# Kernel tuning notes

Measured on AMD Instinct MI355X. Metric: run time of the kernel, lower is better.

Reference implementation:

```python
import jax, jax.numpy as jnp
import numpy as np

D_MODEL, D_STATE, D_CONV, D_INNER, DT_RANK = 1024, 16, 4, 2048, 64
BATCH, LENGTH = 4, 2048


def setup_inputs() -> dict:
    key = jax.random.key(0)
    ks = jax.random.split(key, 10)
    dt_init_std = DT_RANK ** -0.5
    # dt_proj bias init: inverse-softplus of dt sampled log-uniform in [dt_min, dt_max]
    dt_min, dt_max, dt_floor = 0.001, 0.1, 1e-4
    u = jax.random.uniform(ks[9], (D_INNER,))
    dt = jnp.clip(jnp.exp(u * (np.log(dt_max) - np.log(dt_min)) + np.log(dt_min)), dt_floor, None)
    b_dt = dt + jnp.log(-jnp.expm1(-dt))
    return {
        "x": jax.random.normal(ks[0], (BATCH, LENGTH, D_MODEL), jnp.float32),
        "W_in": jax.random.normal(ks[1], (2 * D_INNER, D_MODEL), jnp.float32) * D_MODEL ** -0.5,
        "conv_w": jax.random.normal(ks[2], (D_INNER, 1, D_CONV), jnp.float32) * D_CONV ** -0.5,
        "conv_b": jax.random.normal(ks[3], (D_INNER,), jnp.float32) * 0.01,
        "W_x": jax.random.normal(ks[4], (DT_RANK + 2 * D_STATE, D_INNER), jnp.float32) * D_INNER ** -0.5,
        "W_dt": jax.random.uniform(ks[5], (D_INNER, DT_RANK), jnp.float32, -dt_init_std, dt_init_std),
        "b_dt": b_dt.astype(jnp.float32),
        "A_raw": jax.random.normal(ks[6], (D_STATE, D_INNER), jnp.float32),
        "D": jax.random.normal(ks[7], (D_INNER,), jnp.float32),
        "W_out": jax.random.normal(ks[8], (D_MODEL, D_INNER), jnp.float32) * D_INNER ** -0.5,
    }


def _mamba_fwd(x, W_in, conv_w, conv_b, W_x, W_dt, b_dt, A_raw, D, W_out):
    b, l, _ = x.shape
    d_inner = W_in.shape[0] // 2
    d_state = A_raw.shape[0]
    dt_rank = W_dt.shape[1]
    xz = jnp.einsum('bld,ed->ble', x, W_in)            # (b, l, 2*d_inner)
    xc, z = jnp.split(xz, 2, axis=-1)
    # causal depthwise conv (torch pads both sides by d_conv-1 then keeps first l == left pad)
    xc = xc.transpose(0, 2, 1)                          # (b, d, l)
    k = conv_w.shape[-1]
    xc = jax.lax.conv_general_dilated(
        xc, conv_w, (1,), [(k - 1, 0)],
        dimension_numbers=('NCH', 'OIH', 'NCH'),
        feature_group_count=d_inner) + conv_b[None, :, None]
    xc = jax.nn.silu(xc).transpose(0, 2, 1)             # (b, l, d)
    dbc = jnp.einsum('bld,ed->ble', xc, W_x)            # (b, l, dt_rank+2*d_state)
    dt, B, C = jnp.split(dbc, [dt_rank, dt_rank + d_state], axis=-1)
    delta = jax.nn.softplus(jnp.einsum('blr,dr->bld', dt, W_dt) + b_dt)  # (b, l, d)
    A = -jnp.exp(A_raw)                                 # (n, d), negative real

    def step(h, inp):
        x_t, dlt, B_t, C_t = inp                        # (b,d),(b,d),(b,n),(b,n)
        dA = jnp.exp(dlt[:, None, :] * A[None])          # (b, n, d)
        h = dA * h + (dlt[:, None, :] * B_t[:, :, None]) * x_t[:, None, :]
        y_t = jnp.einsum('bn,bnd->bd', C_t, h) + D * x_t
        return h, y_t

    h0 = jnp.zeros((b, d_state, d_inner), x.dtype)
    xs = (xc.transpose(1, 0, 2), delta.transpose(1, 0, 2),
          B.transpose(1, 0, 2), C.transpose(1, 0, 2))
    _, ys = jax.lax.scan(step, h0, xs)                  # (l, b, d)
    y = ys.transpose(1, 0, 2) * jax.nn.silu(z)
    return jnp.einsum('bld,md->blm', y, W_out)


def reference(x, W_in, conv_w, conv_b, W_x, W_dt, b_dt, A_raw, D, W_out):
    return _mamba_fwd(x, W_in, conv_w, conv_b, W_x, W_dt, b_dt, A_raw, D, W_out)
```

## Files before the change

### kernel.cpp

```cpp
#include <hip/hip_runtime.h>
#include <hip/hip_bf16.h>

typedef __bf16 bf16;
typedef __bf16 bf16x4 __attribute__((ext_vector_type(4)));
typedef __bf16 bf16x8 __attribute__((ext_vector_type(8)));
typedef float f32x4 __attribute__((ext_vector_type(4)));

__device__ __forceinline__ float fast_exp2(float x) {
#if __has_builtin(__builtin_amdgcn_exp2f)
    return __builtin_amdgcn_exp2f(x);
#else
    return exp2f(x);
#endif
}

__device__ __forceinline__ float fast_log(float x) {
#if __has_builtin(__builtin_amdgcn_logf)
    return __builtin_amdgcn_logf(x) * 0.6931471805599453f;
#else
    return __logf(x);
#endif
}

__device__ __forceinline__ void gload16(bf16* lds, const bf16* g) {
    __builtin_amdgcn_global_load_lds(
        (const __attribute__((address_space(1))) void*)g,
        (__attribute__((address_space(3))) void*)lds,
        16, 0, 0);
}

__device__ __forceinline__ bf16x8 cvt8(const float* p) {
    float4 a = *(const float4*)p;
    float4 b = *(const float4*)(p + 4);
    bf16x8 r;
    r[0] = (bf16)a.x; r[1] = (bf16)a.y; r[2] = (bf16)a.z; r[3] = (bf16)a.w;
    r[4] = (bf16)b.x; r[5] = (bf16)b.y; r[6] = (bf16)b.z; r[7] = (bf16)b.w;
    return r;
}

__global__ __launch_bounds__(256) void cvt_bf16(
    const float* __restrict__ in, bf16* __restrict__ out, int n8)
{
    int i = blockIdx.x * 256 + threadIdx.x;
    if (i < n8)
        *(bf16x8*)(out + (size_t)i * 8) = cvt8(in + (size_t)i * 8);
}

__global__ __launch_bounds__(256) void cvt_all(
    const float* __restrict__ x,  const float* __restrict__ W_in,
    const float* __restrict__ W_x, const float* __restrict__ W_dt,
    bf16* __restrict__ xb, bf16* __restrict__ Wlo, bf16* __restrict__ Whi,
    bf16* __restrict__ Wxb, bf16* __restrict__ Wdtb)
{
    int i = blockIdx.x * 256 + threadIdx.x;
    if (i < 1048576) {
        *(bf16x8*)(xb + (size_t)i * 8) = cvt8(x + (size_t)i * 8);
    } else if (i < 1310720) {
        int j = i - 1048576;
        *(bf16x8*)(Wlo + (size_t)j * 8) = cvt8(W_in + (size_t)j * 8);
    } else if (i < 1572864) {
        int j = i - 1310720;
        *(bf16x8*)(Whi + (size_t)j * 8) = cvt8(W_in + 2097152 + (size_t)j * 8);
    } else if (i < 1597440) {
        int j = i - 1572864;
        *(bf16x8*)(Wxb + (size_t)j * 8) = cvt8(W_x + (size_t)j * 8);
    } else if (i < 1613824) {
        int j = i - 1597440;
        *(bf16x8*)(Wdtb + (size_t)j * 8) = cvt8(W_dt + (size_t)j * 8);
    }
}

template <int EPI, typename TC>
__global__ __launch_bounds__(256, 2) void gemm_bt(
    const bf16* __restrict__ A, int lda,
    const bf16* __restrict__ B, int ldb,
    TC* __restrict__ C, int ldc,
    int K, int Neff, const float* __restrict__ bias,
    const bf16* __restrict__ gmul, size_t zstride)
{
    __shared__ bf16 As0[128 * 32];
    __shared__ bf16 As1[128 * 32];
    __shared__ bf16 Bs0[128 * 32];
    __shared__ bf16 Bs1[128 * 32];

    const int tid  = threadIdx.x;
    const int lane = tid & 63;
    const int wave = tid >> 6;
    const int quad = lane >> 4;
    const int l16  = lane & 15;
    const int wm   = (wave >> 1) << 6;
    const int wn   = (wave & 1) << 6;
    const int bm   = blockIdx.x << 7;
    const int bn   = blockIdx.y << 7;
    const int kb   = blockIdx.z * K;

    const int srow = (wave << 4) + (lane >> 2);
    const int scol = (lane & 3) << 3;

    const bf16* Ag0 = A + (size_t)(bm + srow) * lda + kb + scol;
    const bf16* Ag1 = Ag0 + (size_t)lda * 64;
    int br0 = bn + srow;      br0 = br0 < Neff ? br0 : Neff - 1;
    int br1 = bn + srow + 64; br1 = br1 < Neff ? br1 : Neff - 1;
    const bf16* Bg0 = B + (size_t)br0 * ldb + kb + scol;
    const bf16* Bg1 = B + (size_t)br1 * ldb + kb + scol;

    const int wofs = wave * 512;

    f32x4 acc[4][4] = {};

    for (int k0 = 0; k0 < K; k0 += 64) {
        if (k0) __syncthreads();
        gload16(As0 + wofs,        Ag0 + k0);
        gload16(As0 + 2048 + wofs, Ag1 + k0);
        gload16(Bs0 + wofs,        Bg0 + k0);
        gload16(Bs0 + 2048 + wofs, Bg1 + k0);
        gload16(As1 + wofs,        Ag0 + k0 + 32);
        gload16(As1 + 2048 + wofs, Ag1 + k0 + 32);
        gload16(Bs1 + wofs,        Bg0 + k0 + 32);
        gload16(Bs1 + 2048 + wofs, Bg1 + k0 + 32);
        __syncthreads();

#pragma unroll
        for (int kk = 0; kk < 2; ++kk) {
            const bf16* Ak = kk ? As1 : As0;
            const bf16* Bk = kk ? Bs1 : Bs0;
            bf16x8 af[4], bfr[4];
#pragma unroll
            for (int i = 0; i < 4; ++i) {
                af[i]  = *(const bf16x8*)(Ak + (wm + i * 16 + l16) * 32 + quad * 8);
                bfr[i] = *(const bf16x8*)(Bk + (wn + i * 16 + l16) * 32 + quad * 8);
            }
#pragma unroll
            for (int mi = 0; mi < 4; ++mi)
#pragma unroll
                for (int ni = 0; ni < 4; ++ni)
                    acc[mi][ni] = __builtin_amdgcn_mfma_f32_16x16x32_bf16(
                        af[mi], bfr[ni], acc[mi][ni], 0, 0, 0);
        }
    }

    TC* Cz = C + (size_t)blockIdx.z * zstride;

#pragma unroll
    for (int mi = 0; mi < 4; ++mi) {
        const int row = bm + wm + mi * 16 + quad * 4;
#pragma unroll
        for (int ni = 0; ni < 4; ++ni) {
            const int col = bn + wn + ni * 16 + l16;
            if (col < Neff) {
                float bc = (EPI == 1) ? bias[col] : 0.f;
#pragma unroll
                for (int r = 0; r < 4; ++r) {
                    float v = acc[mi][ni][r];
                    if (EPI == 1) {
                        v += bc;
                        float sp = fast_log(1.f + __expf(v));
                        v = (v > 15.f) ? v : sp;
                    } else if (EPI == 2) {
                        float g = v / (1.f + __expf(-v));
                        v = (float)gmul[(size_t)(row + r) * ldc + col] * g;
                    }
                    Cz[(size_t)(row + r) * ldc + col] = (TC)v;
                }
            }
        }
    }
}

__global__ __launch_bounds__(256) void reduce_split(
    const float* __restrict__ P, bf16* __restrict__ dtb,
    float* __restrict__ BCf)
{
    const size_t base = ((size_t)blockIdx.x * 256 + threadIdx.x) * 4;
    f32x4 s = *(const f32x4*)(P + base);
#pragma unroll
    for (int z = 1; z < 4; ++z) {
        f32x4 p = *(const f32x4*)(P + (size_t)z * 786432 + base);
        s[0] += p[0]; s[1] += p[1]; s[2] += p[2]; s[3] += p[3];
    }
    const int row = (int)(base / 96);
    const int col = (int)(base % 96);
    if (col < 64) {
        bf16x4 o;
        o[0] = (bf16)s[0]; o[1] = (bf16)s[1];
        o[2] = (bf16)s[2]; o[3] = (bf16)s[3];
        *(bf16x4*)(dtb + (size_t)row * 64 + col) = o;
    } else {
        *(f32x4*)(BCf + (size_t)row * 32 + (col - 64)) = s;
    }
}

__global__ __launch_bounds__(256) void conv_kernel(
    const bf16* __restrict__ xh, const float* __restrict__ cw,
    const float* __restrict__ cb, bf16* __restrict__ xc)
{
    const int t0 = blockIdx.x << 3;
    const int b  = blockIdx.y;
    const int d  = threadIdx.x * 8;

    float4 wv[8];
#pragma unroll
    for (int i = 0; i < 8; ++i)
        wv[i] = *(const float4*)(cw + (d + i) * 4);

    float4 cb0 = *(const float4*)(cb + d);
    float4 cb1 = *(const float4*)(cb + d + 4);

    float acc[8][8];
#pragma unroll
    for (int k = 0; k < 8; ++k) {
        acc[k][0] = cb0.x; acc[k][1] = cb0.y; acc[k][2] = cb0.z; acc[k][3] = cb0.w;
        acc[k][4] = cb1.x; acc[k][5] = cb1.y; acc[k][6] = cb1.z; acc[k][7] = cb1.w;
    }

    const bf16* base = xh + ((size_t)b * 2048 + t0) * 2048 + d;

#pragma unroll
    for (int r = 0; r < 11; ++r) {
        const int t_in = t0 - 3 + r;
        if (t_in >= 0) {
            bf16x8 v = *(const bf16x8*)(base + (size_t)(r - 3) * 2048);
            float vf[8];
#pragma unroll
            for (int i = 0; i < 8; ++i) vf[i] = (float)v[i];
#pragma unroll
            for (int j = 0; j < 4; ++j) {
                const int local = r - j;
                if (local >= 0 && local < 8) {
#pragma unroll
                    for (int i = 0; i < 8; ++i) {
                        float w = (j == 0) ? wv[i].x : (j == 1) ? wv[i].y
                                : (j == 2) ? wv[i].z : wv[i].w;
                        acc[local][i] += w * vf[i];
                    }
                }
            }
        }
    }

    bf16* ob = xc + ((size_t)b * 2048 + t0) * 2048 + d;
#pragma unroll
    for (int k = 0; k < 8; ++k) {
        bf16x8 o;
#pragma unroll
        for (int i = 0; i < 8; ++i) {
            float s = acc[k][i];
            o[i] = (bf16)(s / (1.f + __expf(-s)));
        }
        *(bf16x8*)(ob + (size_t)k * 2048) = o;
    }
}

__global__ __launch_bounds__(256, 4) void scan_p1(
    const bf16* __restrict__ delta, const float* __restrict__ BCf,
    const float* __restrict__ A_raw, const bf16* __restrict__ xc,
    bf16* __restrict__ Hb, float* __restrict__ sdtb)
{
    const int d = (blockIdx.x << 8) + threadIdx.x;
    const int b = blockIdx.y;
    const int c = blockIdx.z;

    float A2[16];
#pragma unroll
    for (int n = 0; n < 16; ++n)
        A2[n] = -__expf(A_raw[n * 2048 + d]) * 1.44269504f;

    float h[16];
#pragma unroll
    for (int n = 0; n < 16; ++n) h[n] = 0.f;
    float sdt = 0.f;

    const size_t xbase = ((size_t)(b * 2048 + c * 32)) * 2048 + d;
    const bf16* xp = xc + xbase;
    const bf16* dp = delta + xbase;
    const float* bp = BCf + (size_t)(b * 2048 + c * 32) * 32;

    bf16 xr = xp[0], dr = dp[0];
    f32x4 B0 = *(const f32x4*)(bp);
    f32x4 B1 = *(const f32x4*)(bp + 4);
    f32x4 B2 = *(const f32x4*)(bp + 8);
    f32x4 B3 = *(const f32x4*)(bp + 12);

#pragma unroll 4
    for (int t = 0; t < 32; ++t) {
        const float x  = (float)xr;
        const float dt = (float)dr;
        const f32x4 Ba = B0, Bb = B1, Bc = B2, Bd = B3;
        if (t < 31) {
            xr = xp[(size_t)(t + 1) * 2048];
            dr = dp[(size_t)(t + 1) * 2048];
            const float* nb = bp + (size_t)(t + 1) * 32;
            B0 = *(const f32x4*)nb;
            B1 = *(const f32x4*)(nb + 4);
            B2 = *(const f32x4*)(nb + 8);
            B3 = *(const f32x4*)(nb + 12);
        }
        const float dx = dt * x;
        sdt += dt;
#pragma unroll
        for (int n = 0; n < 4; ++n) {
            float e = fast_exp2(dt * A2[n]);
            h[n] = e * h[n] + Ba[n] * dx;
        }
#pragma unroll
        for (int n = 0; n < 4; ++n) {
            float e = fast_exp2(dt * A2[n + 4]);
            h[n + 4] = e * h[n + 4] + Bb[n] * dx;
        }
#pragma unroll
        for (int n = 0; n < 4; ++n) {
            float e = fast_exp2(dt * A2[n + 8]);
            h[n + 8] = e * h[n + 8] + Bc[n] * dx;
        }
#pragma unroll
        for (int n = 0; n < 4; ++n) {
            float e = fast_exp2(dt * A2[n + 12]);
            h[n + 12] = e * h[n + 12] + Bd[n] * dx;
        }
    }

    const size_t hbase = (((size_t)b * 64 + c) * 2048 + d) * 16;
    bf16x8 h0, h1;
#pragma unroll
    for (int n = 0; n < 8; ++n) {
        h0[n] = (bf16)h[n];
        h1[n] = (bf16)h[n + 8];
    }
    *(bf16x8*)(Hb + hbase) = h0;
    *(bf16x8*)(Hb + hbase + 8) = h1;
    sdtb[((size_t)b * 64 + c) * 2048 + d] = sdt;
}

__global__ __launch_bounds__(256) void scan_p2(
    bf16* __restrict__ Hb, const float* __restrict__ sdtb,
    const float* __restrict__ A_raw)
{
    const int id  = blockIdx.x * 256 + threadIdx.x;
    const int b   = id >> 15;
    const int rem = id & 32767;
    const int d   = rem >> 4;
    const int n   = rem & 15;

    const float A2 = -__expf(A_raw[n * 2048 + d]) * 1.44269504f;
    const size_t hb = (size_t)b * 64 * 32768 + rem;
    const size_t sb = (size_t)b * 64 * 2048 + d;

    float ht = (float)Hb[hb];
#pragma unroll 4
    for (int c = 1; c < 64; ++c) {
        float Hv = (float)Hb[hb + (size_t)c * 32768];
        float a  = fast_exp2(A2 * sdtb[sb + (size_t)c * 2048]);
        ht = Hv + a * ht;
        Hb[hb + (size_t)c * 32768] = (bf16)ht;
    }
}

__global__ __launch_bounds__(256, 4) void scan_p3(
    const bf16* __restrict__ delta, const float* __restrict__ BCf,
    const float* __restrict__ A_raw, const float* __restrict__ Dvec,
    const bf16* __restrict__ Hb, const bf16* xc, bf16* ry)
{
    const int d = (blockIdx.x << 8) + threadIdx.x;
    const int b = blockIdx.y;
    const int c = blockIdx.z;

    float A2[16];
#pragma unroll
    for (int n = 0; n < 16; ++n)
        A2[n] = -__expf(A_raw[n * 2048 + d]) * 1.44269504f;
    const float Dd = Dvec[d];

    float h[16];
    if (c > 0) {
        const bf16* Hp = Hb + (((size_t)b * 64 + (c - 1)) * 2048 + d) * 16;
        bf16x8 v0 = *(const bf16x8*)Hp;
        bf16x8 v1 = *(const bf16x8*)(Hp + 8);
#pragma unroll
        for (int n = 0; n < 8; ++n) {
            h[n]     = (float)v0[n];
            h[n + 8] = (float)v1[n];
        }
    } else {
#pragma unroll
        for (int n = 0; n < 16; ++n) h[n] = 0.f;
    }

    const size_t xbase = ((size_t)(b * 2048 + c * 32)) * 2048 + d;
    const bf16* xp = xc + xbase;
    const bf16* dp = delta + xbase;
    const float* bp = BCf + (size_t)(b * 2048 + c * 32) * 32;
    bf16* yp = ry + xbase;

    bf16 xr = xp[0], dr = dp[0];
    f32x4 B0 = *(const f32x4*)(bp);
    f32x4 B1 = *(const f32x4*)(bp + 4);
    f32x4 B2 = *(const f32x4*)(bp + 8);
    f32x4 B3 = *(const f32x4*)(bp + 12);
    f32x4 C0 = *(const f32x4*)(bp + 16);
    f32x4 C1 = *(const f32x4*)(bp + 20);
    f32x4 C2 = *(const f32x4*)(bp + 24);
    f32x4 C3 = *(const f32x4*)(bp + 28);

#pragma unroll 4
    for (int t = 0; t < 32; ++t) {
        const float x  = (float)xr;
        const float dt = (float)dr;
        const f32x4 Ba = B0, Bb = B1, Bc = B2, Bd = B3;
        const f32x4 Ca = C0, Cb = C1, Cc = C2, Cd = C3;
        if (t < 31) {
            xr = xp[(size_t)(t + 1) * 2048];
            dr = dp[(size_t)(t + 1) * 2048];
            const float* nb = bp + (size_t)(t + 1) * 32;
            B0 = *(const f32x4*)nb;
            B1 = *(const f32x4*)(nb + 4);
            B2 = *(const f32x4*)(nb + 8);
            B3 = *(const f32x4*)(nb + 12);
            C0 = *(const f32x4*)(nb + 16);
            C1 = *(const f32x4*)(nb + 20);
            C2 = *(const f32x4*)(nb + 24);
            C3 = *(const f32x4*)(nb + 28);
        }
        const float dx = dt * x;
        float y = Dd * x;
#pragma unroll
        for (int n = 0; n < 4; ++n) {
            float e = fast_exp2(dt * A2[n]);
            h[n] = e * h[n] + Ba[n] * dx;
            y += Ca[n] * h[n];
        }
#pragma unroll
        for (int n = 0; n < 4; ++n) {
            float e = fast_exp2(dt * A2[n + 4]);
            h[n + 4] = e * h[n + 4] + Bb[n] * dx;
            y += Cb[n] * h[n + 4];
        }
#pragma unroll
        for (int n = 0; n < 4; ++n) {
            float e = fast_exp2(dt * A2[n + 8]);
            h[n + 8] = e * h[n + 8] + Bc[n] * dx;
            y += Cc[n] * h[n + 8];
        }
#pragma unroll
        for (int n = 0; n < 4; ++n) {
            float e = fast_exp2(dt * A2[n + 12]);
            h[n + 12] = e * h[n + 12] + Bd[n] * dx;
            y += Cd[n] * h[n + 12];
        }
        yp[(size_t)t * 2048] = (bf16)y;
    }
}

extern "C" void kernel_launch(void* const* d_in, const int* in_sizes, int n_in,
                              void* d_out, int out_size, void* d_ws, size_t ws_size,
                              hipStream_t stream)
{
    const float* x      = (const float*)d_in[0];
    const float* W_in   = (const float*)d_in[1];
    const float* conv_w = (const float*)d_in[2];
    const float* conv_b = (const float*)d_in[3];
    const float* W_x    = (const float*)d_in[4];
    const float* W_dt   = (const float*)d_in[5];
    const float* b_dt   = (const float*)d_in[6];
    const float* A_raw  = (const float*)d_in[7];
    const float* Dvec   = (const float*)d_in[8];
    const float* W_out  = (const float*)d_in[9];
    float* out = (float*)d_out;

    char* ws = (char*)d_ws;
    bf16*  buf0   = (bf16*)(ws + 0);
    bf16*  buf1   = (bf16*)(ws + 33554432);
    char*  dob    = (char*)d_out;
    bf16*  dtb    = (bf16*)dob;
    float* BCf    = (float*)(dob + 1048576);
    bf16*  xb1    = (bf16*)(dob + 2097152);
    float* Pbuf   = (float*)(dob + 2097152);
    bf16*  Hb     = (bf16*)(dob + 2097152);
    bf16*  xb2    = (bf16*)(dob + 2097152);
    float* sdtb   = (float*)(dob + 18874368);
    bf16*  Whi    = (bf16*)(dob + 20971520);
    bf16*  Wxb    = (bf16*)(dob + 25165824);
    bf16*  Wdtb   = (bf16*)(dob + 25690112);
    bf16*  Wlo    = buf1;
    bf16*  Woutb  = buf1;

    cvt_all<<<dim3(6304), 256, 0, stream>>>(
        x, W_in, W_x, W_dt, xb1, Wlo, Whi, Wxb, Wdtb);

    gemm_bt<0, bf16><<<dim3(64, 16), 256, 0, stream>>>(
        xb1, 1024, Wlo, 1024, buf0, 2048, 1024, 2048, nullptr, nullptr, 0);
    conv_kernel<<<dim3(256, 4), 256, 0, stream>>>(buf0, conv_w, conv_b, buf1);
    gemm_bt<0, float><<<dim3(64, 1, 4), 256, 0, stream>>>(
        buf1, 2048, Wxb, 2048, Pbuf, 96, 512, 96, nullptr, nullptr, 786432);
    reduce_split<<<dim3(768), 256, 0, stream>>>(Pbuf, dtb, BCf);
    gemm_bt<1, bf16><<<dim3(64, 16), 256, 0, stream>>>(
        dtb, 64, Wdtb, 64, buf0, 2048, 64, 2048, b_dt, nullptr, 0);
    scan_p1<<<dim3(8, 4, 64), 256, 0, stream>>>(
        buf0, BCf, A_raw, buf1, Hb, sdtb);
    scan_p2<<<dim3(512), 256, 0, stream>>>(Hb, sdtb, A_raw);
    scan_p3<<<dim3(8, 4, 64), 256, 0, stream>>>(
        buf0, BCf, A_raw, Dvec, Hb, buf1, buf1);
    cvt_bf16<<<dim3(4096), 256, 0, stream>>>(x, xb2, 1048576);
    gemm_bt<2, bf16><<<dim3(64, 16), 256, 0, stream>>>(
        xb2, 1024, Whi, 1024, buf0, 2048, 1024, 2048, nullptr, buf1, 0);
    cvt_bf16<<<dim3(1024), 256, 0, stream>>>(W_out, Woutb, 262144);
    gemm_bt<0, float><<<dim3(64, 8), 256, 0, stream>>>(
        buf0, 2048, Woutb, 2048, out, 1024, 2048, 1024, nullptr, nullptr, 0);
}
```

Before: 417.3 us.

## Add 256x256-tile double-buffered MFMA GEMM for the two input projections

Adds a new 512-thread GEMM kernel using 256x256 output tiles and a 64-wide K step. It double-buffers A and B tiles in LDS and raises wave priority around the MFMA bursts. It replaces the 128-tile gemm_bt for both W_in projections (x and z halves, including the fused silu-gate epilogue). The larger tiles raise data reuse per LDS load and cut global traffic. The cost is a single wave of 256 blocks using about 128KB of LDS each, so one block per CU. LDS reads are unswizzled, which risks bank conflicts, and epilogue stores are scalar.

```diff
diff --git a/kernel.cpp b/kernel.cpp
--- a/kernel.cpp
+++ b/kernel.cpp
@@ -67,6 +67,107 @@
     } else if (i < 1613824) {
         int j = i - 1597440;
         *(bf16x8*)(Wdtb + (size_t)j * 8) = cvt8(W_dt + (size_t)j * 8);
+    }
+}
+
+template <int EPI, typename TC>
+__global__ __launch_bounds__(512, 2) void gemm256(
+    const bf16* __restrict__ A, int lda,
+    const bf16* __restrict__ B, int ldb,
+    TC* __restrict__ C, int ldc,
+    int K, const bf16* __restrict__ gmul)
+{
+    __shared__ bf16 sA[2][256 * 64];
+    __shared__ bf16 sB[2][256 * 64];
+
+    const int tid  = threadIdx.x;
+    const int lane = tid & 63;
+    const int wave = tid >> 6;
+    const int quad = lane >> 4;
+    const int l16  = lane & 15;
+    const int wr   = wave >> 2;
+    const int wc   = wave & 3;
+    const int bm   = blockIdx.x << 8;
+    const int bn   = blockIdx.y << 8;
+
+    const int srow = wave * 16 + (lane >> 3);
+    const int scol = (lane & 7) * 8;
+
+    f32x4 acc[8][4] = {};
+
+    const int KT = K >> 6;
+
+#define STAGE(pb, u, kt) do {                                              \
+    int kc_ = (kt) * 64; if (kc_ > K - 64) kc_ = K - 64;                   \
+    const int half_ = (u) & 1;                                             \
+    bf16* dst_ = (((u) < 2) ? sA[pb] : sB[pb]) + (half_ * 128 + wave * 16) * 64; \
+    const bf16* src_ = ((u) < 2)                                           \
+        ? A + (size_t)(bm + half_ * 128 + srow) * lda + kc_ + scol         \
+        : B + (size_t)(bn + half_ * 128 + srow) * ldb + kc_ + scol;        \
+    const int ld_ = ((u) < 2) ? lda : ldb;                                 \
+    gload16(dst_, src_);                                                   \
+    gload16(dst_ + 8 * 64, src_ + (size_t)8 * ld_);                        \
+} while (0)
+
+    STAGE(0, 0, 0); STAGE(0, 1, 0); STAGE(0, 2, 0); STAGE(0, 3, 0);
+
+    for (int it = 0; it < KT / 2; ++it) {
+#pragma unroll
+        for (int ph = 0; ph < 8; ++ph) {
+            const int p = ph >> 2;
+            const int q = ph & 3;
+            STAGE(p ^ 1, q, 2 * it + 1 + p);
+            if (q == 0) {
+                asm volatile("s_waitcnt vmcnt(2)" ::: "memory");
+                __builtin_amdgcn_s_barrier();
+            }
+            const int qm = q >> 1, qn = q & 1;
+            bf16x8 af[4][2], bq[2][2];
+            const bf16* Ar = sA[p] + (wr * 128 + qm * 64 + l16) * 64 + quad * 8;
+            const bf16* Br = sB[p] + (wc * 64 + qn * 32 + l16) * 64 + quad * 8;
+#pragma unroll
+            for (int fm = 0; fm < 4; ++fm)
+#pragma unroll
+                for (int ks = 0; ks < 2; ++ks)
+                    af[fm][ks] = *(const bf16x8*)(Ar + fm * 16 * 64 + ks * 32);
+#pragma unroll
+            for (int fn = 0; fn < 2; ++fn)
+#pragma unroll
+                for (int ks = 0; ks < 2; ++ks)
+                    bq[fn][ks] = *(const bf16x8*)(Br + fn * 16 * 64 + ks * 32);
+            __builtin_amdgcn_s_setprio(1);
+#pragma unroll
+            for (int fm = 0; fm < 4; ++fm)
+#pragma unroll
+                for (int fn = 0; fn < 2; ++fn)
+#pragma unroll
+                    for (int ks = 0; ks < 2; ++ks)
+                        acc[qm * 4 + fm][qn * 2 + fn] =
+                            __builtin_amdgcn_mfma_f32_16x16x32_bf16(
+                                af[fm][ks], bq[fn][ks],
+                                acc[qm * 4 + fm][qn * 2 + fn], 0, 0, 0);
+            __builtin_amdgcn_s_setprio(0);
+            if (q == 3) __builtin_amdgcn_s_barrier();
+        }
+    }
+#undef STAGE
+
+#pragma unroll
+    for (int mi = 0; mi < 8; ++mi) {
+        const int row = bm + wr * 128 + mi * 16 + quad * 4;
+#pragma unroll
+        for (int ni = 0; ni < 4; ++ni) {
+            const int col = bn + wc * 64 + ni * 16 + l16;
+#pragma unroll
+            for (int r = 0; r < 4; ++r) {
+                float v = acc[mi][ni][r];
+                if (EPI == 2) {
+                    float g = v / (1.f + __expf(-v));
+                    v = (float)gmul[(size_t)(row + r) * ldc + col] * g;
+                }
+                C[(size_t)(row + r) * ldc + col] = (TC)v;
+            }
+        }
     }
 }
 
@@ -486,8 +587,8 @@
     cvt_all<<<dim3(6304), 256, 0, stream>>>(
         x, W_in, W_x, W_dt, xb1, Wlo, Whi, Wxb, Wdtb);
 
-    gemm_bt<0, bf16><<<dim3(64, 16), 256, 0, stream>>>(
-        xb1, 1024, Wlo, 1024, buf0, 2048, 1024, 2048, nullptr, nullptr, 0);
+    gemm256<0, bf16><<<dim3(32, 8), 512, 0, stream>>>(
+        xb1, 1024, Wlo, 1024, buf0, 2048, 1024, nullptr);
     conv_kernel<<<dim3(256, 4), 256, 0, stream>>>(buf0, conv_w, conv_b, buf1);
     gemm_bt<0, float><<<dim3(64, 1, 4), 256, 0, stream>>>(
         buf1, 2048, Wxb, 2048, Pbuf, 96, 512, 96, nullptr, nullptr, 786432);
@@ -500,8 +601,8 @@
     scan_p3<<<dim3(8, 4, 64), 256, 0, stream>>>(
         buf0, BCf, A_raw, Dvec, Hb, buf1, buf1);
     cvt_bf16<<<dim3(4096), 256, 0, stream>>>(x, xb2, 1048576);
-    gemm_bt<2, bf16><<<dim3(64, 16), 256, 0, stream>>>(
-        xb2, 1024, Whi, 1024, buf0, 2048, 1024, 2048, nullptr, buf1, 0);
+    gemm256<2, bf16><<<dim3(32, 8), 512, 0, stream>>>(
+        xb2, 1024, Whi, 1024, buf0, 2048, 1024, buf1);
     cvt_bf16<<<dim3(1024), 256, 0, stream>>>(W_out, Woutb, 262144);
     gemm_bt<0, float><<<dim3(64, 8), 256, 0, stream>>>(
         buf0, 2048, Woutb, 2048, out, 1024, 2048, 1024, nullptr, nullptr, 0);
```

Result: slower. 446.6 us (+7.0%).
